# Performance work log

Hardware: AMD Instinct MI355X
Metric: run time of the kernel (lower is better)

## Reference

```python
import jax, jax.numpy as jnp
import numpy as np


def setup_inputs() -> dict:
    key = jax.random.key(0)
    ks = jax.random.split(key, 6)
    nt, ne, b, vs = 48, 48, 32, 512
    targets = jax.random.normal(ks[0], (nt, b, vs), dtype=jnp.float32)
    embeddings = jax.random.normal(ks[1], (ne, b, vs), dtype=jnp.float32)
    # torch nn.Linear(2*dim, dim): weight [dim, 2*dim], bias [dim]
    W1 = jax.random.normal(ks[2], (vs, 2 * vs), dtype=jnp.float32) * (1.0 / np.sqrt(2 * vs))
    b1 = jax.random.normal(ks[3], (vs,), dtype=jnp.float32) * 0.01
    # nn.Linear(dim, 1): weight [1, dim], bias [1]
    W2 = jax.random.normal(ks[4], (1, vs), dtype=jnp.float32) * (1.0 / np.sqrt(vs))
    b2 = jax.random.normal(ks[5], (1,), dtype=jnp.float32) * 0.01
    return {"targets": targets, "embeddings": embeddings, "W1": W1, "b1": b1, "W2": W2, "b2": b2}


def reference(targets, embeddings, W1, b1, W2, b2):
    # targets: [nt, b, vs], embeddings: [ne, b, vs]
    # Original: cat(expand(targets), expand(embeddings), dim=3) @ W1^T.
    # Because concat feeds a linear layer, split W1 = [W1a | W1b] and compute
    # the two matmuls on the small tensors, then broadcast-add — same math,
    # no [nt, ne, b, 2*vs] intermediate.
    vs = targets.shape[-1]
    W1a = W1[:, :vs]   # acts on targets half
    W1b = W1[:, vs:]   # acts on embeddings half
    ta = jnp.einsum('tbv,hv->tbh', targets, W1a)      # [nt, b, dim]
    eb = jnp.einsum('nbv,hv->nbh', embeddings, W1b)   # [ne, b, dim]
    h = jnp.tanh(ta[:, None] + eb[None, :] + b1)       # [nt, ne, b, dim]
    out = jnp.einsum('tnbh,h->tnb', h, W2[0]) + b2[0]  # [nt, ne, b]
    return out
```

## Files before the change

kernel.cpp:

```cpp
#include <hip/hip_runtime.h>

typedef float f32x4 __attribute__((ext_vector_type(4)));
typedef short s16x8 __attribute__((ext_vector_type(8)));
typedef short s16x4 __attribute__((ext_vector_type(4)));

#define NT 48
#define NE 48
#define NB 32
#define VS 512

__device__ __forceinline__ unsigned short f2bf(float f) {
  union { float f; unsigned u; } v; v.f = f;
  unsigned u = v.u;
  unsigned r = u + 0x7FFFu + ((u >> 16) & 1u);
  return (unsigned short)(r >> 16);
}

__device__ __forceinline__ float tanhf_fast(float x) {
  float e = __expf(x * 2.0f);
  return 1.0f - 2.0f * __builtin_amdgcn_rcpf(e + 1.0f);
}

__global__ __launch_bounds__(256) void k_gemm(
    const float* __restrict__ targets, const float* __restrict__ embeddings,
    const float* __restrict__ W1, const float* __restrict__ b1,
    float* __restrict__ C) {
  __shared__ short sa[64][40];
  __shared__ short sb[64][40];

  const int bid = blockIdx.x;
  const int mt = bid >> 3;
  const int ht = bid & 7;
  const int m0 = mt * 64, h0 = ht * 64;
  const bool is_ta = (m0 < 1536);
  const float* Abase = is_ta ? (targets + (size_t)m0 * VS)
                             : (embeddings + (size_t)(m0 - 1536) * VS);
  const float* Bbase = W1 + (size_t)h0 * 1024 + (is_ta ? 0 : 512);

  const int tid = threadIdx.x;
  const int lane = tid & 63, w = tid >> 6;
  const int q = lane >> 4, i = lane & 15;

  f32x4 acc[4] = {{0.f,0.f,0.f,0.f},{0.f,0.f,0.f,0.f},{0.f,0.f,0.f,0.f},{0.f,0.f,0.f,0.f}};

  for (int kt = 0; kt < 16; ++kt) {
    const int k0 = kt * 32;
    if (kt) __syncthreads();
#pragma unroll
    for (int r = 0; r < 4; ++r) {
      int f = r * 256 + tid;
      int g = f & 511;
      int row = g >> 3;
      int col4 = (g & 7) << 2;
      const float* src = (f < 512) ? (Abase + (size_t)row * VS + k0 + col4)
                                   : (Bbase + (size_t)row * 1024 + k0 + col4);
      f32x4 v = *(const f32x4*)src;
      s16x4 o;
#pragma unroll
      for (int u = 0; u < 4; ++u) o[u] = (short)f2bf(v[u]);
      short* dst = (f < 512) ? &sa[row][col4] : &sb[row][col4];
      *(s16x4*)dst = o;
    }
    __syncthreads();
    s16x8 av = *(const s16x8*)&sa[16 * w + i][q * 8];
#pragma unroll
    for (int c = 0; c < 4; ++c) {
      s16x8 bv = *(const s16x8*)&sb[c * 16 + i][q * 8];
      acc[c] = __builtin_amdgcn_mfma_f32_16x16x32_bf16(av, bv, acc[c], 0, 0, 0);
    }
  }

#pragma unroll
  for (int c = 0; c < 4; ++c) {
#pragma unroll
    for (int r = 0; r < 4; ++r) {
      int ml = 16 * w + q * 4 + r;
      int hl = c * 16 + i;
      int m = m0 + ml, h = h0 + hl;
      float v = acc[c][r];
      if (is_ta) v += b1[h];
      C[(size_t)m * VS + h] = v;
    }
  }
}

__global__ __launch_bounds__(256) void k_fuse(
    const float* __restrict__ C, const float* __restrict__ W2,
    const float* __restrict__ b2, float* __restrict__ out) {
  __shared__ float sta[16][260];
  __shared__ float seb[16][260];
  __shared__ float w2c[512];
  __shared__ float red[4][16][17];

  const int bid = blockIdx.x;
  const int b = bid / 9;
  const int r9 = bid % 9;
  const int t0 = (r9 / 3) * 16, n0 = (r9 % 3) * 16;

  const int tid = threadIdx.x;
  const int lane = tid & 63, hq = tid >> 6;
  const int i0 = lane & 7, j0 = (lane >> 3) & 7;

  if (tid < 128) *(f32x4*)&w2c[tid * 4] = *(const f32x4*)&W2[tid * 4];

  float a00 = 0.f, a01 = 0.f, a10 = 0.f, a11 = 0.f;

  for (int chunk = 0; chunk < 2; ++chunk) {
    __syncthreads();
#pragma unroll
    for (int r = 0; r < 8; ++r) {
      int f = r * 256 + tid;
      int g = f & 1023;
      int row = g >> 6;
      int col4 = (g & 63) << 2;
      int m = (f < 1024) ? ((t0 + row) * NB + b)
                         : (1536 + (n0 + row) * NB + b);
      f32x4 v = *(const f32x4*)&C[(size_t)m * VS + chunk * 256 + col4];
      float* dst = (f < 1024) ? &sta[row][col4] : &seb[row][col4];
      *(f32x4*)dst = v;
    }
    __syncthreads();

    const int hbase = hq * 64;
#pragma unroll 4
    for (int it = 0; it < 16; ++it) {
      int h = hbase + it * 4;
      f32x4 ta0 = *(const f32x4*)&sta[i0][h];
      f32x4 ta1 = *(const f32x4*)&sta[i0 + 8][h];
      f32x4 eb0 = *(const f32x4*)&seb[j0][h];
      f32x4 eb1 = *(const f32x4*)&seb[j0 + 8][h];
      f32x4 w4  = *(const f32x4*)&w2c[chunk * 256 + h];
#pragma unroll
      for (int u = 0; u < 4; ++u) {
        float ww = w4[u];
        a00 += tanhf_fast(ta0[u] + eb0[u]) * ww;
        a01 += tanhf_fast(ta0[u] + eb1[u]) * ww;
        a10 += tanhf_fast(ta1[u] + eb0[u]) * ww;
        a11 += tanhf_fast(ta1[u] + eb1[u]) * ww;
      }
    }
  }

  red[hq][i0][j0]         = a00;
  red[hq][i0][j0 + 8]     = a01;
  red[hq][i0 + 8][j0]     = a10;
  red[hq][i0 + 8][j0 + 8] = a11;
  __syncthreads();
  {
    int tl = tid & 15, nl = tid >> 4;
    float s = red[0][tl][nl] + red[1][tl][nl] + red[2][tl][nl] + red[3][tl][nl] + b2[0];
    out[((size_t)(t0 + tl) * NE + (n0 + nl)) * NB + b] = s;
  }
}

extern "C" void kernel_launch(void* const* d_in, const int* in_sizes, int n_in,
                              void* d_out, int out_size, void* d_ws, size_t ws_size,
                              hipStream_t stream) {
  (void)in_sizes; (void)n_in; (void)out_size; (void)ws_size;
  const float* targets    = (const float*)d_in[0];
  const float* embeddings = (const float*)d_in[1];
  const float* W1         = (const float*)d_in[2];
  const float* b1         = (const float*)d_in[3];
  const float* W2         = (const float*)d_in[4];
  const float* b2         = (const float*)d_in[5];
  float* out = (float*)d_out;
  float* C   = (float*)d_ws;

  k_gemm<<<dim3(384), dim3(256), 0, stream>>>(targets, embeddings, W1, b1, C);
  k_fuse<<<dim3(288), dim3(256), 0, stream>>>(C, W2, b2, out);
}
```

Before: 116.0 us.

## Precompute exp in GEMM epilogue, factor tanh into product reciprocal, split hidden dim

The GEMM epilogue now stores exp(2x) instead of x. This lets the fuse kernel compute tanh(a+b) as 1 - 2/(e^{2a}·e^{2b}+1), which needs one multiply plus one reciprocal and no per-element exp. The fuse kernel is split across four hidden-dimension quarters with 512-thread blocks, which gives more blocks. Partial sums are combined with atomicAdd into an output that the GEMM kernel zeroes, and a per-quarter constant (sum of W2 plus b2/4) is precomputed. Risks include exp overflow to inf for large pre-activations, atomic contention, and a nondeterministic summation order.

```diff
diff --git a/kernel.cpp b/kernel.cpp
--- a/kernel.cpp
+++ b/kernel.cpp
@@ -1,34 +1,41 @@
 #include <hip/hip_runtime.h>
+#include <hip/hip_bf16.h>
 
 typedef float f32x4 __attribute__((ext_vector_type(4)));
 typedef short s16x8 __attribute__((ext_vector_type(8)));
-typedef short s16x4 __attribute__((ext_vector_type(4)));
 
 #define NT 48
 #define NE 48
 #define NB 32
 #define VS 512
-
-__device__ __forceinline__ unsigned short f2bf(float f) {
-  union { float f; unsigned u; } v; v.f = f;
-  unsigned u = v.u;
-  unsigned r = u + 0x7FFFu + ((u >> 16) & 1u);
-  return (unsigned short)(r >> 16);
-}
-
-__device__ __forceinline__ float tanhf_fast(float x) {
-  float e = __expf(x * 2.0f);
-  return 1.0f - 2.0f * __builtin_amdgcn_rcpf(e + 1.0f);
-}
+#define NOUT (NT * NE * NB)
+#define CX_OFF (3072 * 512)
 
 __global__ __launch_bounds__(256) void k_gemm(
     const float* __restrict__ targets, const float* __restrict__ embeddings,
     const float* __restrict__ W1, const float* __restrict__ b1,
-    float* __restrict__ C) {
+    const float* __restrict__ W2, const float* __restrict__ b2,
+    float* __restrict__ C, float* __restrict__ out) {
   __shared__ short sa[64][40];
   __shared__ short sb[64][40];
 
   const int bid = blockIdx.x;
+  const int tid = threadIdx.x;
+
+  {
+    int zi = bid * 256 + tid;
+    if (zi < NOUT) out[zi] = 0.0f;
+  }
+  if (bid == 0 && tid < 64) {
+#pragma unroll
+    for (int q = 0; q < 4; ++q) {
+      float s = W2[q * 128 + tid] + W2[q * 128 + 64 + tid];
+#pragma unroll
+      for (int off = 32; off; off >>= 1) s += __shfl_xor(s, off, 64);
+      if (tid == 0) C[CX_OFF + q] = 0.25f * b2[0] + s;
+    }
+  }
+
   const int mt = bid >> 3;
   const int ht = bid & 7;
   const int m0 = mt * 64, h0 = ht * 64;
@@ -37,7 +44,6 @@
                              : (embeddings + (size_t)(m0 - 1536) * VS);
   const float* Bbase = W1 + (size_t)h0 * 1024 + (is_ta ? 0 : 512);
 
-  const int tid = threadIdx.x;
   const int lane = tid & 63, w = tid >> 6;
   const int q = lane >> 4, i = lane & 15;
 
@@ -55,11 +61,12 @@
       const float* src = (f < 512) ? (Abase + (size_t)row * VS + k0 + col4)
                                    : (Bbase + (size_t)row * 1024 + k0 + col4);
       f32x4 v = *(const f32x4*)src;
-      s16x4 o;
-#pragma unroll
-      for (int u = 0; u < 4; ++u) o[u] = (short)f2bf(v[u]);
+      union { __hip_bfloat162 h2; unsigned u; } c0, c1;
+      c0.h2 = __float22bfloat162_rn(float2{v[0], v[1]});
+      c1.h2 = __float22bfloat162_rn(float2{v[2], v[3]});
+      uint2 o; o.x = c0.u; o.y = c1.u;
       short* dst = (f < 512) ? &sa[row][col4] : &sb[row][col4];
-      *(s16x4*)dst = o;
+      *(uint2*)dst = o;
     }
     __syncthreads();
     s16x8 av = *(const s16x8*)&sa[16 * w + i][q * 8];
@@ -79,77 +86,80 @@
       int m = m0 + ml, h = h0 + hl;
       float v = acc[c][r];
       if (is_ta) v += b1[h];
-      C[(size_t)m * VS + h] = v;
+      C[(size_t)m * VS + h] = __expf(v + v);
     }
   }
 }
 
-__global__ __launch_bounds__(256) void k_fuse(
+__global__ __launch_bounds__(512) void k_fuse(
     const float* __restrict__ C, const float* __restrict__ W2,
-    const float* __restrict__ b2, float* __restrict__ out) {
-  __shared__ float sta[16][260];
-  __shared__ float seb[16][260];
-  __shared__ float w2c[512];
-  __shared__ float red[4][16][17];
+    float* __restrict__ out) {
+  __shared__ float sta[16][132];
+  __shared__ float seb[16][132];
+  __shared__ float w2c[128];
+  __shared__ float red[8][16][17];
 
   const int bid = blockIdx.x;
-  const int b = bid / 9;
-  const int r9 = bid % 9;
-  const int t0 = (r9 / 3) * 16, n0 = (r9 % 3) * 16;
+  const int b = bid & 31;
+  const int r5 = bid >> 5;
+  const int hq = r5 & 3;
+  const int r2 = r5 >> 2;
+  const int t0 = (r2 / 3) * 16, n0 = (r2 % 3) * 16;
 
   const int tid = threadIdx.x;
-  const int lane = tid & 63, hq = tid >> 6;
+
+#pragma unroll
+  for (int rr = 0; rr < 2; ++rr) {
+    int f = rr * 512 + tid;
+    int g = f & 511;
+    int row = g >> 5;
+    int col4 = (g & 31) << 2;
+    int m = (f < 512) ? ((t0 + row) * NB + b)
+                      : (1536 + (n0 + row) * NB + b);
+    f32x4 v = *(const f32x4*)&C[(size_t)m * VS + hq * 128 + col4];
+    float* dst = (f < 512) ? &sta[row][col4] : &seb[row][col4];
+    *(f32x4*)dst = v;
+  }
+  if (tid < 32) *(f32x4*)&w2c[tid * 4] = *(const f32x4*)&W2[hq * 128 + tid * 4];
+  __syncthreads();
+
+  const int w = tid >> 6, lane = tid & 63;
   const int i0 = lane & 7, j0 = (lane >> 3) & 7;
-
-  if (tid < 128) *(f32x4*)&w2c[tid * 4] = *(const f32x4*)&W2[tid * 4];
+  const int hb = w * 16;
 
   float a00 = 0.f, a01 = 0.f, a10 = 0.f, a11 = 0.f;
-
-  for (int chunk = 0; chunk < 2; ++chunk) {
-    __syncthreads();
 #pragma unroll
-    for (int r = 0; r < 8; ++r) {
-      int f = r * 256 + tid;
-      int g = f & 1023;
-      int row = g >> 6;
-      int col4 = (g & 63) << 2;
-      int m = (f < 1024) ? ((t0 + row) * NB + b)
-                         : (1536 + (n0 + row) * NB + b);
-      f32x4 v = *(const f32x4*)&C[(size_t)m * VS + chunk * 256 + col4];
-      float* dst = (f < 1024) ? &sta[row][col4] : &seb[row][col4];
-      *(f32x4*)dst = v;
-    }
-    __syncthreads();
-
-    const int hbase = hq * 64;
-#pragma unroll 4
-    for (int it = 0; it < 16; ++it) {
-      int h = hbase + it * 4;
-      f32x4 ta0 = *(const f32x4*)&sta[i0][h];
-      f32x4 ta1 = *(const f32x4*)&sta[i0 + 8][h];
-      f32x4 eb0 = *(const f32x4*)&seb[j0][h];
-      f32x4 eb1 = *(const f32x4*)&seb[j0 + 8][h];
-      f32x4 w4  = *(const f32x4*)&w2c[chunk * 256 + h];
+  for (int it = 0; it < 4; ++it) {
+    int h = hb + it * 4;
+    f32x4 et0 = *(const f32x4*)&sta[i0][h];
+    f32x4 et1 = *(const f32x4*)&sta[i0 + 8][h];
+    f32x4 en0 = *(const f32x4*)&seb[j0][h];
+    f32x4 en1 = *(const f32x4*)&seb[j0 + 8][h];
+    f32x4 w4  = *(const f32x4*)&w2c[h];
 #pragma unroll
-      for (int u = 0; u < 4; ++u) {
-        float ww = w4[u];
-        a00 += tanhf_fast(ta0[u] + eb0[u]) * ww;
-        a01 += tanhf_fast(ta0[u] + eb1[u]) * ww;
-        a10 += tanhf_fast(ta1[u] + eb0[u]) * ww;
-        a11 += tanhf_fast(ta1[u] + eb1[u]) * ww;
-      }
+    for (int u = 0; u < 4; ++u) {
+      float r00 = __builtin_amdgcn_rcpf(et0[u] * en0[u] + 1.0f);
+      float r01 = __builtin_amdgcn_rcpf(et0[u] * en1[u] + 1.0f);
+      float r10 = __builtin_amdgcn_rcpf(et1[u] * en0[u] + 1.0f);
+      float r11 = __builtin_amdgcn_rcpf(et1[u] * en1[u] + 1.0f);
+      float ww = w4[u];
+      a00 += ww * r00; a01 += ww * r01; a10 += ww * r10; a11 += ww * r11;
     }
   }
 
-  red[hq][i0][j0]         = a00;
-  red[hq][i0][j0 + 8]     = a01;
-  red[hq][i0 + 8][j0]     = a10;
-  red[hq][i0 + 8][j0 + 8] = a11;
+  red[w][i0][j0]         = a00;
+  red[w][i0][j0 + 8]     = a01;
+  red[w][i0 + 8][j0]     = a10;
+  red[w][i0 + 8][j0 + 8] = a11;
   __syncthreads();
-  {
+
+  if (tid < 256) {
     int tl = tid & 15, nl = tid >> 4;
-    float s = red[0][tl][nl] + red[1][tl][nl] + red[2][tl][nl] + red[3][tl][nl] + b2[0];
-    out[((size_t)(t0 + tl) * NE + (n0 + nl)) * NB + b] = s;
+    float s = 0.f;
+#pragma unroll
+    for (int ww = 0; ww < 8; ++ww) s += red[ww][tl][nl];
+    float val = C[CX_OFF + hq] - 2.0f * s;
+    atomicAdd(&out[((size_t)(t0 + tl) * NE + (n0 + nl)) * NB + b], val);
   }
 }
 
@@ -166,6 +176,6 @@
   float* out = (float*)d_out;
   float* C   = (float*)d_ws;
 
-  k_gemm<<<dim3(384), dim3(256), 0, stream>>>(targets, embeddings, W1, b1, C);
-  k_fuse<<<dim3(288), dim3(256), 0, stream>>>(C, W2, b2, out);
+  k_gemm<<<dim3(384), dim3(256), 0, stream>>>(targets, embeddings, W1, b1, W2, b2, C, out);
+  k_fuse<<<dim3(1152), dim3(512), 0, stream>>>(C, W2, out);
 }
```

New measurement: 103.9 us. 10.4% less time.
